# Optimization experiments

Hardware: AMD Instinct MI355X
Metric: run time of the kernel (lower is better)

Reference implementation:

```python
import jax, jax.numpy as jnp
import numpy as np

B, S, D, H = 1, 4096, 768, 12
W_HEAD = D // H  # 64


def setup_inputs() -> dict:
    key = jax.random.key(0)
    k1, k2, k3 = jax.random.split(key, 3)
    x = jax.random.normal(k1, (B, S, D), dtype=jnp.float32)
    mask = jnp.ones((B, S), dtype=jnp.float32)
    W_qkv = jax.random.normal(k2, (D, 3 * D), dtype=jnp.float32) * (1.0 / np.sqrt(D))
    b_qkv = jax.random.normal(k3, (3 * D,), dtype=jnp.float32) * 0.02
    return {"x": x, "mask": mask, "W_qkv": W_qkv, "b_qkv": b_qkv}


def reference(x, mask, W_qkv, b_qkv):
    # fused QKV projection: (B,S,D) @ (D,3D) -> (B,S,3D)
    qkv = jnp.einsum('bsd,de->bse', x, W_qkv) + b_qkv
    q, k, v = jnp.split(qkv, 3, axis=-1)
    # split heads: (B,S,D) -> (B,H,S,W)
    def to_heads(t):
        return t.reshape(B, S, H, W_HEAD).transpose(0, 2, 1, 3)
    q, k, v = to_heads(q), to_heads(k), to_heads(v)
    scores = jnp.einsum('bhsw,bhtw->bhst', q, k) / np.sqrt(W_HEAD)
    # additive mask: mask (B,S) -> (B,1,1,S); 1 = keep
    scores = scores - 10000.0 * (1.0 - mask[:, None, None, :])
    scores = jax.nn.softmax(scores, axis=-1)
    h = jnp.einsum('bhst,bhtw->bhsw', scores, v)
    # merge heads: (B,H,S,W) -> (B,S,D)
    h = h.transpose(0, 2, 1, 3).reshape(B, S, D)
    return h
```

## Files before the change

### kernel.cpp

```cpp
#include <hip/hip_runtime.h>
#include <hip/hip_bf16.h>

namespace {
constexpr int S  = 4096;
constexpr int D  = 768;
constexpr int H  = 12;
constexpr int N3 = 2304;

typedef __bf16 bf16x4 __attribute__((ext_vector_type(4)));
typedef __bf16 bf16x8 __attribute__((ext_vector_type(8)));
typedef float  floatx4 __attribute__((ext_vector_type(4)));

__device__ inline void glds16(const __bf16* g, __bf16* l) {
  __builtin_amdgcn_global_load_lds(
      (const __attribute__((address_space(1))) void*)(const void*)g,
      (__attribute__((address_space(3))) void*)(void*)l, 16, 0, 0);
}

__global__ __launch_bounds__(256)
void convert_all(const float* __restrict__ x, __bf16* __restrict__ xb,
                 const float* __restrict__ W, __bf16* __restrict__ WT)
{
  const int bid = blockIdx.x;
  const int tid = threadIdx.x;
  if (bid < 3072) {
    const int i = (bid * 256 + tid) * 4;
    floatx4 v = *reinterpret_cast<const floatx4*>(x + i);
    bf16x4 b;
    #pragma unroll
    for (int e = 0; e < 4; ++e) b[e] = (__bf16)v[e];
    *reinterpret_cast<bf16x4*>(xb + i) = b;
  } else {
    __shared__ float T[64][65];
    const int b2 = bid - 3072;
    const int d0 = (b2 % 12) * 64, e0 = (b2 / 12) * 64;
    const int rr = tid >> 4, c4 = (tid & 15) * 4;
    #pragma unroll
    for (int it = 0; it < 4; ++it) {
      int d = it * 16 + rr;
      floatx4 v = *reinterpret_cast<const floatx4*>(W + (d0 + d) * N3 + e0 + c4);
      #pragma unroll
      for (int e = 0; e < 4; ++e) T[d][c4 + e] = v[e];
    }
    __syncthreads();
    #pragma unroll
    for (int it = 0; it < 4; ++it) {
      int e = it * 16 + rr;
      bf16x4 b;
      #pragma unroll
      for (int i = 0; i < 4; ++i) b[i] = (__bf16)T[c4 + i][e];
      *reinterpret_cast<bf16x4*>(WT + (e0 + e) * D + d0 + c4) = b;
    }
  }
}

__global__ __launch_bounds__(256)
void qkv_gemm(const __bf16* __restrict__ xb, const __bf16* __restrict__ WT,
              const float* __restrict__ bq, __bf16* __restrict__ Qb,
              __bf16* __restrict__ Kb, __bf16* __restrict__ vT)
{
  __shared__ __bf16 smem[14336];
  const int tid  = threadIdx.x;
  const int wave = tid >> 6, lane = tid & 63;
  const int quad = lane >> 4, l16 = lane & 15;
  const int m_base = (wave >> 1) * 64;
  const int n_base = (wave & 1) * 48;
  const int bm = blockIdx.x, bn = blockIdx.y;

  floatx4 acc[4][3];
  #pragma unroll
  for (int i = 0; i < 4; ++i)
    #pragma unroll
    for (int j = 0; j < 3; ++j) acc[i][j] = (floatx4){0.f, 0.f, 0.f, 0.f};

  auto stageA = [&](int k, int h) {
    #pragma unroll
    for (int it = 0; it < 2; ++it) {
      int r0 = it * 64 + wave * 16;
      int row = r0 + (lane >> 2);
      glds16(xb + (size_t)(bm * 128 + row) * D + k * 32
                + (((lane & 3) ^ ((row >> 1) & 3)) * 8),
             smem + h * 4096 + r0 * 32);
    }
  };
  auto stageB = [&](int k, int h) {
    #pragma unroll
    for (int it = 0; it < 2; ++it) {
      int r0 = it * 64 + wave * 16;
      if (r0 < 96) {
        int row = r0 + (lane >> 2);
        glds16(WT + (size_t)(bn * 96 + row) * D + k * 32
                  + (((lane & 3) ^ ((row >> 1) & 3)) * 8),
               smem + 8192 + h * 3072 + r0 * 32);
      }
    }
  };

  __builtin_amdgcn_sched_barrier(0);
  stageA(0, 0); stageB(0, 0);
  __builtin_amdgcn_sched_barrier(0);

  for (int k = 0; k < 24; ++k) {
    const int h = k & 1;
    asm volatile("s_waitcnt vmcnt(0)" ::: "memory");
    __builtin_amdgcn_s_barrier();
    __builtin_amdgcn_sched_barrier(0);

    if (k < 23) { stageA(k + 1, h ^ 1); stageB(k + 1, h ^ 1); }
    __builtin_amdgcn_sched_barrier(0);

    bf16x8 af[4], bfr[3];
    #pragma unroll
    for (int mt = 0; mt < 4; ++mt) {
      int m = m_base + mt * 16 + l16;
      af[mt] = *reinterpret_cast<const bf16x8*>(
          &smem[h * 4096 + m * 32 + ((quad ^ ((m >> 1) & 3)) << 3)]);
    }
    #pragma unroll
    for (int nt = 0; nt < 3; ++nt) {
      int n = n_base + nt * 16 + l16;
      bfr[nt] = *reinterpret_cast<const bf16x8*>(
          &smem[8192 + h * 3072 + n * 32 + ((quad ^ ((n >> 1) & 3)) << 3)]);
    }
    #pragma unroll
    for (int mt = 0; mt < 4; ++mt)
      #pragma unroll
      for (int nt = 0; nt < 3; ++nt)
        acc[mt][nt] = __builtin_amdgcn_mfma_f32_16x16x32_bf16(
            af[mt], bfr[nt], acc[mt][nt], 0, 0, 0);
  }

  if (bn < 16) {
    #pragma unroll
    for (int nt = 0; nt < 3; ++nt) {
      int col = bn * 96 + n_base + nt * 16 + l16;
      float bias = bq[col];
      #pragma unroll
      for (int mt = 0; mt < 4; ++mt) {
        int row = bm * 128 + m_base + mt * 16 + quad * 4;
        #pragma unroll
        for (int r = 0; r < 4; ++r) {
          __bf16 v = (__bf16)(acc[mt][nt][r] + bias);
          if (bn < 8) Qb[(row + r) * D + col] = v;
          else        Kb[(row + r) * D + (col - D)] = v;
        }
      }
    }
  } else {
    __syncthreads();
    __bf16* vts = smem;
    #pragma unroll
    for (int nt = 0; nt < 3; ++nt) {
      int wl = n_base + nt * 16 + l16;
      float bias = bq[bn * 96 + wl];
      int sw = (wl & 7) << 3;
      #pragma unroll
      for (int mt = 0; mt < 4; ++mt) {
        #pragma unroll
        for (int r = 0; r < 4; ++r) {
          int tl = m_base + mt * 16 + quad * 4 + r;
          int pos = (tl & ~31) | (quad << 3) | ((tl & 16) >> 2) | r;
          vts[wl * 128 + (pos ^ sw)] = (__bf16)(acc[mt][nt][r] + bias);
        }
      }
    }
    __syncthreads();
    const int w0g = bn * 96 - 2 * D;
    #pragma unroll
    for (int it = 0; it < 6; ++it) {
      int c = it * 256 + tid;
      int wl = c >> 4, t0 = (c & 15) * 8;
      bf16x8 v = *reinterpret_cast<const bf16x8*>(
          &vts[wl * 128 + (t0 ^ ((wl & 7) << 3))]);
      *reinterpret_cast<bf16x8*>(
          &vT[(size_t)(w0g + wl) * S + bm * 128 + t0]) = v;
    }
  }
}

__global__ __launch_bounds__(256)
void attention(const __bf16* __restrict__ Qb, const __bf16* __restrict__ Kb,
               const __bf16* __restrict__ vT, const float* __restrict__ mask,
               float* __restrict__ out)
{
  __shared__ char smem[49408];
  __bf16* Vt = (__bf16*)(smem + 32768);
  float*  Ll = (float*)(smem + 49152);
  float*  Lo = (float*)smem;

  const int tid  = threadIdx.x;
  const int wave = tid >> 6, lane = tid & 63;
  const int quad = lane >> 4, l16 = lane & 15;
  const int qh = wave >> 1;
  const int th = wave & 1;
  const int qb = blockIdx.x, h = blockIdx.y;
  const int q0 = qb * 64;
  const int qcol = h * 64;
  const int srow = lane >> 3, sg = lane & 7;
  const int vrow = lane >> 4, vs = lane & 15;

  bf16x8 qf[2][2];
  #pragma unroll
  for (int nt = 0; nt < 2; ++nt)
    #pragma unroll
    for (int kt = 0; kt < 2; ++kt)
      qf[nt][kt] = *reinterpret_cast<const bf16x8*>(
          Qb + (q0 + qh * 32 + nt * 16 + l16) * D + qcol + kt * 32 + quad * 8);

  floatx4 accO[4][2];
  #pragma unroll
  for (int wt = 0; wt < 4; ++wt)
    #pragma unroll
    for (int nt = 0; nt < 2; ++nt) accO[wt][nt] = (floatx4){0.f, 0.f, 0.f, 0.f};
  floatx4 accL[2];
  accL[0] = (floatx4){0.f, 0.f, 0.f, 0.f};
  accL[1] = (floatx4){0.f, 0.f, 0.f, 0.f};
  bf16x8 ones;
  #pragma unroll
  for (int e = 0; e < 8; ++e) ones[e] = (__bf16)1.0f;

  auto stageK = [&](int j, __bf16* dst) {
    #pragma unroll
    for (int it = 0; it < 4; ++it) {
      int rbase = it * 32 + wave * 8;
      int t = rbase + srow;
      glds16(Kb + (size_t)(j * 128 + t) * D + qcol + (sg ^ (t & 7)) * 8,
             dst + rbase * 64);
    }
  };
  auto stageV = [&](int j) {
    #pragma unroll
    for (int it = 0; it < 4; ++it) {
      int wbase = it * 16 + wave * 4;
      int w = wbase + vrow;
      glds16(vT + (size_t)(qcol + w) * S + j * 128 + (vs ^ (w & 7)) * 8,
             Vt + wbase * 128);
    }
  };

  stageK(0, (__bf16*)smem);
  stageV(0);

  for (int j = 0; j < 32; ++j) {
    floatx4 mv[4];
    #pragma unroll
    for (int mt = 0; mt < 4; ++mt)
      mv[mt] = *reinterpret_cast<const floatx4*>(
          mask + j * 128 + th * 64 + mt * 16 + quad * 4);

    asm volatile("s_waitcnt vmcnt(8)" ::: "memory");
    __builtin_amdgcn_s_barrier();
    __builtin_amdgcn_sched_barrier(0);

    if (j < 31)
      stageK(j + 1, (__bf16*)(smem + (((j + 1) & 1) << 14)));
    __builtin_amdgcn_sched_barrier(0);

    const __bf16* Kc = (const __bf16*)(smem + ((j & 1) << 14));

    bf16x8 pf[2][2];
    #pragma unroll
    for (int mt = 0; mt < 4; ++mt) {
      int trow = th * 64 + mt * 16 + l16;
      bf16x8 kf[2];
      #pragma unroll
      for (int kt = 0; kt < 2; ++kt)
        kf[kt] = *reinterpret_cast<const bf16x8*>(
            &Kc[trow * 64 + ((((kt << 2) | quad) ^ (l16 & 7)) << 3)]);
      floatx4 am;
      #pragma unroll
      for (int r = 0; r < 4; ++r)
        am[r] = fmaf(mv[mt][r], 14426.9504f, -14426.9504f);
      #pragma unroll
      for (int nt = 0; nt < 2; ++nt) {
        floatx4 s = (floatx4){0.f, 0.f, 0.f, 0.f};
        #pragma unroll
        for (int kt = 0; kt < 2; ++kt)
          s = __builtin_amdgcn_mfma_f32_16x16x32_bf16(kf[kt], qf[nt][kt], s, 0, 0, 0);
        #pragma unroll
        for (int r = 0; r < 4; ++r)
          pf[mt >> 1][nt][(mt & 1) * 4 + r] = (__bf16)__builtin_amdgcn_exp2f(
              fmaf(s[r], 0.18033688f, am[r]));
      }
    }

    asm volatile("s_waitcnt vmcnt(4)" ::: "memory");
    __builtin_amdgcn_s_barrier();
    __builtin_amdgcn_sched_barrier(0);

    __builtin_amdgcn_s_setprio(1);
    #pragma unroll
    for (int u = 0; u < 2; ++u) {
      #pragma unroll
      for (int nt = 0; nt < 2; ++nt)
        accL[nt] = __builtin_amdgcn_mfma_f32_16x16x32_bf16(
            ones, pf[u][nt], accL[nt], 0, 0, 0);
      #pragma unroll
      for (int wt = 0; wt < 4; ++wt) {
        int w = wt * 16 + l16;
        bf16x8 vf = *reinterpret_cast<const bf16x8*>(
            &Vt[w * 128 + (((th * 8 + u * 4 + quad) ^ (w & 7)) << 3)]);
        #pragma unroll
        for (int nt = 0; nt < 2; ++nt)
          accO[wt][nt] = __builtin_amdgcn_mfma_f32_16x16x32_bf16(
              vf, pf[u][nt], accO[wt][nt], 0, 0, 0);
      }
    }
    __builtin_amdgcn_s_setprio(0);

    __builtin_amdgcn_s_barrier();
    __builtin_amdgcn_sched_barrier(0);
    if (j < 31) stageV(j + 1);
    __builtin_amdgcn_sched_barrier(0);
  }

  float l_lane[2] = {accL[0][0], accL[1][0]};

  __syncthreads();
  if (th == 1) {
    float* dst = Lo + qh * (64 * 33);
    #pragma unroll
    for (int wt = 0; wt < 4; ++wt)
      #pragma unroll
      for (int nt = 0; nt < 2; ++nt)
        #pragma unroll
        for (int r = 0; r < 4; ++r)
          dst[(wt * 16 + quad * 4 + r) * 33 + nt * 16 + l16] = accO[wt][nt][r];
    if (quad == 0) {
      #pragma unroll
      for (int nt = 0; nt < 2; ++nt)
        Ll[qh * 32 + nt * 16 + l16] = l_lane[nt];
    }
  }
  __syncthreads();
  if (th == 0) {
    const float* src = Lo + qh * (64 * 33);
    float l_tot[2];
    #pragma unroll
    for (int nt = 0; nt < 2; ++nt)
      l_tot[nt] = l_lane[nt] + Ll[qh * 32 + nt * 16 + l16];
    #pragma unroll
    for (int wt = 0; wt < 4; ++wt)
      #pragma unroll
      for (int nt = 0; nt < 2; ++nt) {
        floatx4 o;
        #pragma unroll
        for (int r = 0; r < 4; ++r)
          o[r] = (accO[wt][nt][r] +
                  src[(wt * 16 + quad * 4 + r) * 33 + nt * 16 + l16]) / l_tot[nt];
        int row = q0 + qh * 32 + nt * 16 + l16;
        int col = qcol + wt * 16 + quad * 4;
        *reinterpret_cast<floatx4*>(&out[row * D + col]) = o;
      }
  }
}

}

extern "C" void kernel_launch(void* const* d_in, const int* in_sizes, int n_in,
                              void* d_out, int out_size, void* d_ws, size_t ws_size,
                              hipStream_t stream) {
  const float *x = nullptr, *mask = nullptr, *Wq = nullptr, *bq = nullptr;
  for (int i = 0; i < n_in; ++i) {
    switch (in_sizes[i]) {
      case 3145728: x    = (const float*)d_in[i]; break;
      case 4096:    mask = (const float*)d_in[i]; break;
      case 1769472: Wq   = (const float*)d_in[i]; break;
      case 2304:    bq   = (const float*)d_in[i]; break;
      default: break;
    }
  }

  __bf16* xb = (__bf16*)d_out;
  __bf16* WT = xb + (size_t)S * D;
  __bf16* Qb = (__bf16*)d_ws;
  __bf16* Kb = Qb + (size_t)S * D;
  __bf16* vT = Kb + (size_t)S * D;

  convert_all<<<3072 + 432, 256, 0, stream>>>(x, xb, Wq, WT);
  qkv_gemm   <<<dim3(S / 128, N3 / 96), 256, 0, stream>>>(xb, WT, bq, Qb, Kb, vT);
  attention  <<<dim3(S / 64, H), 256, 0, stream>>>(Qb, Kb, vT, mask, (float*)d_out);
}
```

Measured before the change: 165.1 us.

## Fuse convert, QKV GEMM and attention into one cooperative persistent kernel

```diff
diff --git a/kernel.cpp b/kernel.cpp
--- a/kernel.cpp
+++ b/kernel.cpp
@@ -1,5 +1,8 @@
 #include <hip/hip_runtime.h>
 #include <hip/hip_bf16.h>
+#include <hip/hip_cooperative_groups.h>
+
+namespace cg = cooperative_groups;
 
 namespace {
 constexpr int S  = 4096;
@@ -15,6 +18,344 @@
   __builtin_amdgcn_global_load_lds(
       (const __attribute__((address_space(1))) void*)(const void*)g,
       (__attribute__((address_space(3))) void*)(void*)l, 16, 0, 0);
+}
+
+__global__ __launch_bounds__(256, 3)
+void fused_all(const float* __restrict__ x, const float* __restrict__ mask,
+               const float* __restrict__ W, const float* __restrict__ bq,
+               float* __restrict__ out, __bf16* __restrict__ Qb,
+               __bf16* __restrict__ Kb, __bf16* __restrict__ vT)
+{
+  __shared__ char smem[49408];
+  const int bid = blockIdx.x;
+  const int tid = threadIdx.x;
+  __bf16* xb = (__bf16*)out;
+  __bf16* WT = xb + (size_t)S * D;
+
+  {
+    #pragma unroll
+    for (int it = 0; it < 4; ++it) {
+      int i = (it * 196608 + bid * 256 + tid) * 4;
+      floatx4 v = *reinterpret_cast<const floatx4*>(x + i);
+      bf16x4 b;
+      #pragma unroll
+      for (int e = 0; e < 4; ++e) b[e] = (__bf16)v[e];
+      *reinterpret_cast<bf16x4*>(xb + i) = b;
+    }
+    if (bid < 432) {
+      float* T = (float*)smem;
+      const int d0 = (bid % 12) * 64, e0 = (bid / 12) * 64;
+      const int rr = tid >> 4, c4 = (tid & 15) * 4;
+      #pragma unroll
+      for (int it = 0; it < 4; ++it) {
+        int d = it * 16 + rr;
+        floatx4 v = *reinterpret_cast<const floatx4*>(W + (d0 + d) * N3 + e0 + c4);
+        #pragma unroll
+        for (int e = 0; e < 4; ++e) T[d * 65 + c4 + e] = v[e];
+      }
+      __syncthreads();
+      #pragma unroll
+      for (int it = 0; it < 4; ++it) {
+        int e = it * 16 + rr;
+        bf16x4 b;
+        #pragma unroll
+        for (int i2 = 0; i2 < 4; ++i2) b[i2] = (__bf16)T[(c4 + i2) * 65 + e];
+        *reinterpret_cast<bf16x4*>(WT + (e0 + e) * D + d0 + c4) = b;
+      }
+    }
+  }
+  cg::this_grid().sync();
+
+  {
+    __bf16* gs = (__bf16*)smem;
+    const int wave = tid >> 6, lane = tid & 63;
+    const int quad = lane >> 4, l16 = lane & 15;
+    const int m_base = (wave >> 1) * 64;
+    const int n_base = (wave & 1) * 48;
+    const int bm = bid & 31, bn = bid >> 5;
+
+    floatx4 acc[4][3];
+    #pragma unroll
+    for (int i = 0; i < 4; ++i)
+      #pragma unroll
+      for (int j = 0; j < 3; ++j) acc[i][j] = (floatx4){0.f, 0.f, 0.f, 0.f};
+
+    auto stageA = [&](int k, int h) {
+      #pragma unroll
+      for (int it = 0; it < 2; ++it) {
+        int r0 = it * 64 + wave * 16;
+        int row = r0 + (lane >> 2);
+        glds16(xb + (size_t)(bm * 128 + row) * D + k * 32
+                  + (((lane & 3) ^ ((row >> 1) & 3)) * 8),
+               gs + h * 4096 + r0 * 32);
+      }
+    };
+    auto stageB = [&](int k, int h) {
+      #pragma unroll
+      for (int it = 0; it < 2; ++it) {
+        int r0 = it * 64 + wave * 16;
+        if (r0 < 96) {
+          int row = r0 + (lane >> 2);
+          glds16(WT + (size_t)(bn * 96 + row) * D + k * 32
+                    + (((lane & 3) ^ ((row >> 1) & 3)) * 8),
+                 gs + 8192 + h * 3072 + r0 * 32);
+        }
+      }
+    };
+
+    __builtin_amdgcn_sched_barrier(0);
+    stageA(0, 0); stageB(0, 0);
+    __builtin_amdgcn_sched_barrier(0);
+
+    for (int k = 0; k < 24; ++k) {
+      const int h = k & 1;
+      asm volatile("s_waitcnt vmcnt(0)" ::: "memory");
+      __builtin_amdgcn_s_barrier();
+      __builtin_amdgcn_sched_barrier(0);
+
+      if (k < 23) { stageA(k + 1, h ^ 1); stageB(k + 1, h ^ 1); }
+      __builtin_amdgcn_sched_barrier(0);
+
+      bf16x8 af[4], bfr[3];
+      #pragma unroll
+      for (int mt = 0; mt < 4; ++mt) {
+        int m = m_base + mt * 16 + l16;
+        af[mt] = *reinterpret_cast<const bf16x8*>(
+            &gs[h * 4096 + m * 32 + ((quad ^ ((m >> 1) & 3)) << 3)]);
+      }
+      #pragma unroll
+      for (int nt = 0; nt < 3; ++nt) {
+        int n = n_base + nt * 16 + l16;
+        bfr[nt] = *reinterpret_cast<const bf16x8*>(
+            &gs[8192 + h * 3072 + n * 32 + ((quad ^ ((n >> 1) & 3)) << 3)]);
+      }
+      #pragma unroll
+      for (int mt = 0; mt < 4; ++mt)
+        #pragma unroll
+        for (int nt = 0; nt < 3; ++nt)
+          acc[mt][nt] = __builtin_amdgcn_mfma_f32_16x16x32_bf16(
+              af[mt], bfr[nt], acc[mt][nt], 0, 0, 0);
+    }
+
+    if (bn < 16) {
+      #pragma unroll
+      for (int nt = 0; nt < 3; ++nt) {
+        int col = bn * 96 + n_base + nt * 16 + l16;
+        float bias = bq[col];
+        #pragma unroll
+        for (int mt = 0; mt < 4; ++mt) {
+          int row = bm * 128 + m_base + mt * 16 + quad * 4;
+          #pragma unroll
+          for (int r = 0; r < 4; ++r) {
+            __bf16 v = (__bf16)(acc[mt][nt][r] + bias);
+            if (bn < 8) Qb[(row + r) * D + col] = v;
+            else        Kb[(row + r) * D + (col - D)] = v;
+          }
+        }
+      }
+    } else {
+      __syncthreads();
+      __bf16* vts = gs;
+      #pragma unroll
+      for (int nt = 0; nt < 3; ++nt) {
+        int wl = n_base + nt * 16 + l16;
+        float bias = bq[bn * 96 + wl];
+        int sw = (wl & 7) << 3;
+        #pragma unroll
+        for (int mt = 0; mt < 4; ++mt) {
+          #pragma unroll
+          for (int r = 0; r < 4; ++r) {
+            int tl = m_base + mt * 16 + quad * 4 + r;
+            int pos = (tl & ~31) | (quad << 3) | ((tl & 16) >> 2) | r;
+            vts[wl * 128 + (pos ^ sw)] = (__bf16)(acc[mt][nt][r] + bias);
+          }
+        }
+      }
+      __syncthreads();
+      const int w0g = bn * 96 - 2 * D;
+      #pragma unroll
+      for (int it = 0; it < 6; ++it) {
+        int c = it * 256 + tid;
+        int wl = c >> 4, t0 = (c & 15) * 8;
+        bf16x8 v = *reinterpret_cast<const bf16x8*>(
+            &vts[wl * 128 + (t0 ^ ((wl & 7) << 3))]);
+        *reinterpret_cast<bf16x8*>(
+            &vT[(size_t)(w0g + wl) * S + bm * 128 + t0]) = v;
+      }
+    }
+  }
+  cg::this_grid().sync();
+
+  {
+    __bf16* Vt = (__bf16*)(smem + 32768);
+    float*  Ll = (float*)(smem + 49152);
+    float*  Lo = (float*)smem;
+
+    const int wave = tid >> 6, lane = tid & 63;
+    const int quad = lane >> 4, l16 = lane & 15;
+    const int qh = wave >> 1;
+    const int th = wave & 1;
+    const int qb = bid & 63, h = bid >> 6;
+    const int q0 = qb * 64;
+    const int qcol = h * 64;
+    const int srow = lane >> 3, sg = lane & 7;
+    const int vrow = lane >> 4, vs = lane & 15;
+
+    bf16x8 qf[2][2];
+    #pragma unroll
+    for (int nt = 0; nt < 2; ++nt)
+      #pragma unroll
+      for (int kt = 0; kt < 2; ++kt)
+        qf[nt][kt] = *reinterpret_cast<const bf16x8*>(
+            Qb + (q0 + qh * 32 + nt * 16 + l16) * D + qcol + kt * 32 + quad * 8);
+
+    floatx4 accO[4][2];
+    #pragma unroll
+    for (int wt = 0; wt < 4; ++wt)
+      #pragma unroll
+      for (int nt = 0; nt < 2; ++nt) accO[wt][nt] = (floatx4){0.f, 0.f, 0.f, 0.f};
+    floatx4 accL[2];
+    accL[0] = (floatx4){0.f, 0.f, 0.f, 0.f};
+    accL[1] = (floatx4){0.f, 0.f, 0.f, 0.f};
+    bf16x8 ones;
+    #pragma unroll
+    for (int e = 0; e < 8; ++e) ones[e] = (__bf16)1.0f;
+
+    auto stageK = [&](int j, __bf16* dst) {
+      #pragma unroll
+      for (int it = 0; it < 4; ++it) {
+        int rbase = it * 32 + wave * 8;
+        int t = rbase + srow;
+        glds16(Kb + (size_t)(j * 128 + t) * D + qcol + (sg ^ (t & 7)) * 8,
+               dst + rbase * 64);
+      }
+    };
+    auto stageV = [&](int j) {
+      #pragma unroll
+      for (int it = 0; it < 4; ++it) {
+        int wbase = it * 16 + wave * 4;
+        int w = wbase + vrow;
+        glds16(vT + (size_t)(qcol + w) * S + j * 128 + (vs ^ (w & 7)) * 8,
+               Vt + wbase * 128);
+      }
+    };
+
+    stageK(0, (__bf16*)smem);
+    stageV(0);
+
+    for (int j = 0; j < 32; ++j) {
+      floatx4 mv[4];
+      #pragma unroll
+      for (int mt = 0; mt < 4; ++mt)
+        mv[mt] = *reinterpret_cast<const floatx4*>(
+            mask + j * 128 + th * 64 + mt * 16 + quad * 4);
+
+      asm volatile("s_waitcnt vmcnt(8)" ::: "memory");
+      __builtin_amdgcn_s_barrier();
+      __builtin_amdgcn_sched_barrier(0);
+
+      if (j < 31)
+        stageK(j + 1, (__bf16*)(smem + (((j + 1) & 1) << 14)));
+      __builtin_amdgcn_sched_barrier(0);
+
+      const __bf16* Kc = (const __bf16*)(smem + ((j & 1) << 14));
+
+      bf16x8 pf[2][2];
+      #pragma unroll
+      for (int mt = 0; mt < 4; ++mt) {
+        int trow = th * 64 + mt * 16 + l16;
+        bf16x8 kf[2];
+        #pragma unroll
+        for (int kt = 0; kt < 2; ++kt)
+          kf[kt] = *reinterpret_cast<const bf16x8*>(
+              &Kc[trow * 64 + ((((kt << 2) | quad) ^ (l16 & 7)) << 3)]);
+        floatx4 am;
+        #pragma unroll
+        for (int r = 0; r < 4; ++r)
+          am[r] = fmaf(mv[mt][r], 14426.9504f, -14426.9504f);
+        #pragma unroll
+        for (int nt = 0; nt < 2; ++nt) {
+          floatx4 s = (floatx4){0.f, 0.f, 0.f, 0.f};
+          #pragma unroll
+          for (int kt = 0; kt < 2; ++kt)
+            s = __builtin_amdgcn_mfma_f32_16x16x32_bf16(kf[kt], qf[nt][kt], s, 0, 0, 0);
+          #pragma unroll
+          for (int r = 0; r < 4; ++r)
+            pf[mt >> 1][nt][(mt & 1) * 4 + r] = (__bf16)__builtin_amdgcn_exp2f(
+                fmaf(s[r], 0.18033688f, am[r]));
+        }
+      }
+
+      asm volatile("s_waitcnt vmcnt(4)" ::: "memory");
+      __builtin_amdgcn_s_barrier();
+      __builtin_amdgcn_sched_barrier(0);
+
+      __builtin_amdgcn_s_setprio(1);
+      #pragma unroll
+      for (int u = 0; u < 2; ++u) {
+        #pragma unroll
+        for (int nt = 0; nt < 2; ++nt)
+          accL[nt] = __builtin_amdgcn_mfma_f32_16x16x32_bf16(
+              ones, pf[u][nt], accL[nt], 0, 0, 0);
+        #pragma unroll
+        for (int wt = 0; wt < 4; ++wt) {
+          int w = wt * 16 + l16;
+          bf16x8 vf = *reinterpret_cast<const bf16x8*>(
+              &Vt[w * 128 + (((th * 8 + u * 4 + quad) ^ (w & 7)) << 3)]);
+          #pragma unroll
+          for (int nt = 0; nt < 2; ++nt)
+            accO[wt][nt] = __builtin_amdgcn_mfma_f32_16x16x32_bf16(
+                vf, pf[u][nt], accO[wt][nt], 0, 0, 0);
+        }
+      }
+      __builtin_amdgcn_s_setprio(0);
+
+      __builtin_amdgcn_s_barrier();
+      __builtin_amdgcn_sched_barrier(0);
+      if (j < 31) stageV(j + 1);
+      __builtin_amdgcn_sched_barrier(0);
+    }
+
+    float l_lane[2] = {accL[0][0], accL[1][0]};
+
+    __syncthreads();
+    if (th == 1) {
+      float* dst = Lo + qh * (64 * 33);
+      #pragma unroll
+      for (int wt = 0; wt < 4; ++wt)
+        #pragma unroll
+        for (int nt = 0; nt < 2; ++nt)
+          #pragma unroll
+          for (int r = 0; r < 4; ++r)
+            dst[(wt * 16 + quad * 4 + r) * 33 + nt * 16 + l16] = accO[wt][nt][r];
+      if (quad == 0) {
+        #pragma unroll
+        for (int nt = 0; nt < 2; ++nt)
+          Ll[qh * 32 + nt * 16 + l16] = l_lane[nt];
+      }
+    }
+    __syncthreads();
+    if (th == 0) {
+      const float* src = Lo + qh * (64 * 33);
+      float l_tot[2];
+      #pragma unroll
+      for (int nt = 0; nt < 2; ++nt)
+        l_tot[nt] = l_lane[nt] + Ll[qh * 32 + nt * 16 + l16];
+      #pragma unroll
+      for (int wt = 0; wt < 4; ++wt)
+        #pragma unroll
+        for (int nt = 0; nt < 2; ++nt) {
+          floatx4 o;
+          #pragma unroll
+          for (int r = 0; r < 4; ++r)
+            o[r] = (accO[wt][nt][r] +
+                    src[(wt * 16 + quad * 4 + r) * 33 + nt * 16 + l16]) / l_tot[nt];
+          int row = q0 + qh * 32 + nt * 16 + l16;
+          int col = qcol + wt * 16 + quad * 4;
+          *reinterpret_cast<floatx4*>(&out[row * D + col]) = o;
+        }
+    }
+  }
 }
 
 __global__ __launch_bounds__(256)
@@ -376,8 +717,24 @@
   __bf16* Qb = (__bf16*)d_ws;
   __bf16* Kb = Qb + (size_t)S * D;
   __bf16* vT = Kb + (size_t)S * D;
-
-  convert_all<<<3072 + 432, 256, 0, stream>>>(x, xb, Wq, WT);
-  qkv_gemm   <<<dim3(S / 128, N3 / 96), 256, 0, stream>>>(xb, WT, bq, Qb, Kb, vT);
-  attention  <<<dim3(S / 64, H), 256, 0, stream>>>(Qb, Kb, vT, mask, (float*)d_out);
+  float*  outp = (float*)d_out;
+
+  static int coop_ok = -1;
+  if (coop_ok < 0) {
+    int nb = 0;
+    if (hipOccupancyMaxActiveBlocksPerMultiprocessor(
+            &nb, (const void*)fused_all, 256, 0) != hipSuccess) nb = 0;
+    coop_ok = (nb >= 3) ? 1 : 0;
+  }
+
+  if (coop_ok) {
+    void* kargs[] = {(void*)&x, (void*)&mask, (void*)&Wq, (void*)&bq,
+                     (void*)&outp, (void*)&Qb, (void*)&Kb, (void*)&vT};
+    hipLaunchCooperativeKernel((const void*)fused_all, dim3(768), dim3(256),
+                               kargs, 0, stream);
+  } else {
+    convert_all<<<3072 + 432, 256, 0, stream>>>(x, xb, Wq, WT);
+    qkv_gemm   <<<dim3(S / 128, N3 / 96), 256, 0, stream>>>(xb, WT, bq, Qb, Kb, vT);
+    attention  <<<dim3(S / 64, H), 256, 0, stream>>>(Qb, Kb, vT, mask, (float*)d_out);
+  }
 }
```

Result: no change. 166.2 us (+0.7%).
